# Performance work log

Hardware: AMD Instinct MI355X
Metric: run time of the kernel (lower is better)

## Reference

```python
import jax, jax.numpy as jnp
import numpy as np

# Module hyperparameters (from init_kwargs)
B, KP, H = 64, 21, 256          # batch, keypoints, heatmap size
KS, SIGMA = 9, 1.5              # Gaussian kernel size / sigma
PAD = KS // 2


def _gaussian_kernel2d(ksize, sigma):
    # matches cv2.getGaussianKernel(ksize, sigma) @ its transpose
    xs = np.arange(ksize, dtype=np.float64) - (ksize - 1) / 2.0
    g = np.exp(-(xs ** 2) / (2.0 * sigma ** 2))
    g /= g.sum()
    return (np.outer(g, g)).astype(np.float32)


def setup_inputs() -> dict:
    key = jax.random.key(0)
    # integer pixel coordinates (row, col) in [0, H)
    x = jax.random.randint(key, (B, KP, 2), 0, H, dtype=jnp.int32)
    kernel2d = jnp.asarray(_gaussian_kernel2d(KS, SIGMA))
    return {"x": x, "kernel2d": kernel2d}


def reference(x, kernel2d):
    # scatter: bg[b, k, crd0, crd1] = 10  (one point per (b, k), no duplicates)
    crd = x.reshape(-1, 2)                       # [B*KP, 2]
    flat = jnp.arange(B * KP)
    b_idx, k_idx = flat // KP, flat % KP
    bg = jnp.zeros((B, KP, H, H), jnp.float32)
    bg = bg.at[b_idx, k_idx, crd[:, 0], crd[:, 1]].set(10.0)

    # block-diagonal conv == depthwise conv with the shared Gaussian patch
    w = jnp.broadcast_to(kernel2d[None, None], (KP, 1, KS, KS))
    out = jax.lax.conv_general_dilated(
        bg, w,
        window_strides=(1, 1),
        padding=[(PAD, PAD), (PAD, PAD)],
        dimension_numbers=("NCHW", "OIHW", "NCHW"),
        feature_group_count=KP,
    )
    return out
```

## Files before the change

### kernel.cpp

```cpp
#include <hip/hip_runtime.h>

#define BB   64
#define KP   21
#define HH   256
#define KS   9
#define PADK 4

__global__ void heatmap_patch_kernel(const int* __restrict__ x,
                                     const float* __restrict__ k2d,
                                     float* __restrict__ out) {
    const int p = blockIdx.x;
    const int t = threadIdx.x;
    if (t >= KS * KS) return;

    const int r = x[2 * p];
    const int c = x[2 * p + 1];

    const int dy = t / KS;
    const int dx = t - dy * KS;
    const int i = r - PADK + dy;
    const int j = c - PADK + dx;
    if (i < 0 || i >= HH || j < 0 || j >= HH) return;

    const float v = 10.0f * k2d[(KS - 1 - dy) * KS + (KS - 1 - dx)];
    out[(size_t)p * (HH * HH) + (size_t)i * HH + j] = v;
}

extern "C" void kernel_launch(void* const* d_in, const int* in_sizes, int n_in,
                              void* d_out, int out_size, void* d_ws, size_t ws_size,
                              hipStream_t stream) {
    const int*   x    = (const int*)d_in[0];
    const float* k2d  = (const float*)d_in[1];
    float*       out  = (float*)d_out;

    hipMemsetAsync(out, 0, (size_t)out_size * sizeof(float), stream);

    heatmap_patch_kernel<<<BB * KP, 128, 0, stream>>>(x, k2d, out);
}
```

Before: 63.01 us.

## Fuse zero-fill and Gaussian patch write into one vectorized kernel

Replaces the memset followed by a scatter kernel with a single kernel. It writes every output float4 once, either zero or the Gaussian patch values computed inline. This removes the separate memset pass and the second kernel launch with its scattered writes. In exchange, every element now pays a bounds check, and the write throughput must match the tuned memset.

```diff
diff --git a/kernel.cpp b/kernel.cpp
--- a/kernel.cpp
+++ b/kernel.cpp
@@ -6,34 +6,54 @@
 #define KS   9
 #define PADK 4
 
-__global__ void heatmap_patch_kernel(const int* __restrict__ x,
-                                     const float* __restrict__ k2d,
-                                     float* __restrict__ out) {
-    const int p = blockIdx.x;
-    const int t = threadIdx.x;
-    if (t >= KS * KS) return;
+#define NPLANES          (BB * KP)
+#define F4_PER_PLANE     (HH * HH / 4)
+#define BLOCKS_PER_PLANE 4
+#define THREADS          256
+#define F4_PER_THREAD    (F4_PER_PLANE / (BLOCKS_PER_PLANE * THREADS))
+
+__global__ __launch_bounds__(THREADS)
+void heatmap_fused_kernel(const int* __restrict__ x,
+                          const float* __restrict__ k2d,
+                          float4* __restrict__ out) {
+    const int p   = blockIdx.x / BLOCKS_PER_PLANE;
+    const int sub = blockIdx.x % BLOCKS_PER_PLANE;
+    const int t   = threadIdx.x;
 
     const int r = x[2 * p];
     const int c = x[2 * p + 1];
 
-    const int dy = t / KS;
-    const int dx = t - dy * KS;
-    const int i = r - PADK + dy;
-    const int j = c - PADK + dx;
-    if (i < 0 || i >= HH || j < 0 || j >= HH) return;
+    float4* plane = out + (size_t)p * F4_PER_PLANE;
+    const float4 z = make_float4(0.f, 0.f, 0.f, 0.f);
 
-    const float v = 10.0f * k2d[(KS - 1 - dy) * KS + (KS - 1 - dx)];
-    out[(size_t)p * (HH * HH) + (size_t)i * HH + j] = v;
+#pragma unroll
+    for (int ch = 0; ch < F4_PER_THREAD; ++ch) {
+        const int f4   = sub * (F4_PER_PLANE / BLOCKS_PER_PLANE) + ch * THREADS + t;
+        const int i    = f4 >> 6;
+        const int col0 = (f4 & 63) << 2;
+
+        float4 v = z;
+        if (i >= r - PADK && i <= r + PADK &&
+            col0 + 3 >= c - PADK && col0 <= c + PADK) {
+            const int di = r - i + PADK;
+            float vals[4];
+#pragma unroll
+            for (int e = 0; e < 4; ++e) {
+                const int dj = c - (col0 + e) + PADK;
+                vals[e] = (dj >= 0 && dj < KS) ? 10.0f * k2d[di * KS + dj] : 0.0f;
+            }
+            v = make_float4(vals[0], vals[1], vals[2], vals[3]);
+        }
+        plane[f4] = v;
+    }
 }
 
 extern "C" void kernel_launch(void* const* d_in, const int* in_sizes, int n_in,
                               void* d_out, int out_size, void* d_ws, size_t ws_size,
                               hipStream_t stream) {
-    const int*   x    = (const int*)d_in[0];
-    const float* k2d  = (const float*)d_in[1];
-    float*       out  = (float*)d_out;
+    const int*   x   = (const int*)d_in[0];
+    const float* k2d = (const float*)d_in[1];
+    float4*      out = (float4*)d_out;
 
-    hipMemsetAsync(out, 0, (size_t)out_size * sizeof(float), stream);
-
-    heatmap_patch_kernel<<<BB * KP, 128, 0, stream>>>(x, k2d, out);
+    heatmap_fused_kernel<<<NPLANES * BLOCKS_PER_PLANE, THREADS, 0, stream>>>(x, k2d, out);
 }
```

New measurement: 69.49 us. 1.1x slower.
